# Kernel tuning notes

Hardware: AMD Instinct MI355X
Metric: run time of the kernel (lower is better)

## Reference

```python
import jax, jax.numpy as jnp
import numpy as np

BETA = 0.25

def setup_inputs() -> dict:
    key = jax.random.key(0)
    k1, k2 = jax.random.split(key)
    N, K, D = 262144, 256, 256
    z_e = jax.random.normal(k1, (N, D), dtype=jnp.float32)
    # nn.Embedding init: uniform(-1/K, 1/K)
    emb_weight = jax.random.uniform(k2, (K, D), dtype=jnp.float32, minval=-1.0 / K, maxval=1.0 / K)
    return {"z_e": z_e, "emb_weight": emb_weight}

def reference(z_e, emb_weight):
    # squared L2 distances: ||z||^2 + ||e||^2 - 2 z e^T  -> [N, K]
    dist = (jnp.sum(z_e ** 2, axis=1, keepdims=True)
            + jnp.sum(emb_weight ** 2, axis=1)
            - 2.0 * jnp.matmul(z_e, emb_weight.T))
    encoding_inds = jnp.argmin(dist, axis=1)  # [N]
    z_q = emb_weight[encoding_inds]           # [N, D]

    sg = jax.lax.stop_gradient
    commitment_loss = jnp.mean((sg(z_e) - z_q) ** 2)
    codebook_loss = jnp.mean((z_e - sg(z_q)) ** 2)
    loss = codebook_loss + BETA * commitment_loss

    # straight-through estimator
    z_q_st = z_e + sg(z_q - z_e)
    return z_q_st, encoding_inds, loss
```

## Files before the change

### kernel.cpp

```cpp
#include <hip/hip_runtime.h>

typedef __attribute__((ext_vector_type(8))) short bf16x8;
typedef __attribute__((ext_vector_type(4))) float f32x4;
typedef __attribute__((ext_vector_type(4))) unsigned short us4;
typedef __attribute__((ext_vector_type(8))) unsigned short us8;

#define NROWS 262144
#define KC 256
#define DD 256
#define BM 64
#define DK 32
#define SW 40
#define TAU 1.5e-3f
#define FCAP 65536

__device__ __forceinline__ float np_pw128_sq(const float* a) {
    float r[8];
#pragma unroll
    for (int j = 0; j < 8; ++j) r[j] = __fmul_rn(a[j], a[j]);
    for (int i = 8; i < 128; i += 8) {
#pragma unroll
        for (int j = 0; j < 8; ++j)
            r[j] = __fadd_rn(r[j], __fmul_rn(a[i + j], a[i + j]));
    }
    float t01 = __fadd_rn(r[0], r[1]), t23 = __fadd_rn(r[2], r[3]);
    float t45 = __fadd_rn(r[4], r[5]), t67 = __fadd_rn(r[6], r[7]);
    return __fadd_rn(__fadd_rn(t01, t23), __fadd_rn(t45, t67));
}
__device__ __forceinline__ float np_sum256_sq(const float* a) {
    return __fadd_rn(np_pw128_sq(a), np_pw128_sq(a + 128));
}

__device__ __forceinline__ unsigned short bf16_rne(float x) {
    unsigned b = __float_as_uint(x);
    b += 0x7FFFu + ((b >> 16) & 1u);
    return (unsigned short)(b >> 16);
}

__global__ void vq_prep(const float* __restrict__ emb, float* __restrict__ se,
                        double* __restrict__ accum, int* __restrict__ gcnt) {
    int k = threadIdx.x;
    if (k == 0) { *accum = 0.0; *gcnt = 0; }
    se[k] = np_sum256_sq(emb + (size_t)k * DD);
}

__global__ void vq_split(const float* __restrict__ emb, unsigned short* __restrict__ ph) {
    int f = (blockIdx.x * 256 + threadIdx.x) * 4;
    float4 v = *reinterpret_cast<const float4*>(emb + f);
    int k = f >> 8, d = f & 255;
    int off = (d >> 5) * (KC * DK) + k * DK + (d & 31);
    us4 h;
    h[0] = bf16_rne(v.x); h[1] = bf16_rne(v.y);
    h[2] = bf16_rne(v.z); h[3] = bf16_rne(v.w);
    *reinterpret_cast<us4*>(ph + off) = h;
}

__global__ __launch_bounds__(256)
void vq_main(const float* __restrict__ ze, const float* __restrict__ emb,
             const unsigned short* __restrict__ ph,
             const float* __restrict__ se_g, float* __restrict__ out_zq,
             float* __restrict__ out_inds, double* __restrict__ accum,
             int* __restrict__ glist, int* __restrict__ gcnt)
{
    __shared__ __attribute__((aligned(16))) unsigned short es_hi[KC * SW];
    __shared__ float  se_s[KC];
    __shared__ int    inds_s[BM];
    __shared__ float  red[256];

    const int t = threadIdx.x;
    const int w = t >> 6;
    const int l = t & 63;
    const int q = (t >> 4) & 3;
    const int c = t & 15;
    const size_t m0 = (size_t)blockIdx.x * BM;

    se_s[t] = se_g[t];

    const unsigned short* ehp0 = ph;
    us8 ereg[4];
#pragma unroll
    for (int it = 0; it < 4; ++it)
        ereg[it] = *reinterpret_cast<const us8*>(ehp0 + (it * 256 + t) * 8);

    const float* zrow = ze + (m0 + 16 * w + c) * DD + q * 8;
    float4 zlo[8], zhi[8];
#pragma unroll
    for (int dci = 0; dci < 8; ++dci) {
        zlo[dci] = *reinterpret_cast<const float4*>(zrow + dci * 32);
        zhi[dci] = *reinterpret_cast<const float4*>(zrow + dci * 32 + 4);
    }

    float sz_acc = 0.f;
    bf16x8 afrag[8];
#pragma unroll
    for (int dci = 0; dci < 8; ++dci) {
        float4 a = zlo[dci], b = zhi[dci];
        sz_acc = fmaf(a.x, a.x, sz_acc); sz_acc = fmaf(a.y, a.y, sz_acc);
        sz_acc = fmaf(a.z, a.z, sz_acc); sz_acc = fmaf(a.w, a.w, sz_acc);
        sz_acc = fmaf(b.x, b.x, sz_acc); sz_acc = fmaf(b.y, b.y, sz_acc);
        sz_acc = fmaf(b.z, b.z, sz_acc); sz_acc = fmaf(b.w, b.w, sz_acc);
        us8 h;
        h[0] = bf16_rne(a.x); h[1] = bf16_rne(a.y); h[2] = bf16_rne(a.z); h[3] = bf16_rne(a.w);
        h[4] = bf16_rne(b.x); h[5] = bf16_rne(b.y); h[6] = bf16_rne(b.z); h[7] = bf16_rne(b.w);
        afrag[dci] = __builtin_bit_cast(bf16x8, h);
    }

#pragma unroll
    for (int it = 0; it < 4; ++it) {
        int idx = it * 256 + t;
        *reinterpret_cast<us8*>(&es_hi[(idx >> 2) * SW + (idx & 3) * 8]) = ereg[it];
    }

    f32x4 acc[16];
#pragma unroll
    for (int i = 0; i < 16; ++i) acc[i] = (f32x4){0.f, 0.f, 0.f, 0.f};

#pragma unroll
    for (int dci = 0; dci < 8; ++dci) {
        __syncthreads();
        if (dci < 7) {
            const unsigned short* ehp = ph + (dci + 1) * (KC * DK);
#pragma unroll
            for (int it = 0; it < 4; ++it)
                ereg[it] = *reinterpret_cast<const us8*>(ehp + (it * 256 + t) * 8);
        }
#pragma unroll
        for (int nf = 0; nf < 16; ++nf) {
            bf16x8 b = *reinterpret_cast<const bf16x8*>(&es_hi[(16 * nf + c) * SW + q * 8]);
            acc[nf] = __builtin_amdgcn_mfma_f32_16x16x32_bf16(afrag[dci], b, acc[nf], 0, 0, 0);
        }
        __syncthreads();
        if (dci < 7) {
#pragma unroll
            for (int it = 0; it < 4; ++it) {
                int idx = it * 256 + t;
                *reinterpret_cast<us8*>(&es_hi[(idx >> 2) * SW + (idx & 3) * 8]) = ereg[it];
            }
        }
    }

    float lossv = 0.f;
#pragma unroll
    for (int j = 0; j < 4; ++j) {
        float v1 = 3.4e38f, v2 = 3.4e38f; int k1 = 0x7fffffff;
#pragma unroll
        for (int nf = 0; nf < 16; ++nf) {
            int k = 16 * nf + c;
            float dv = fmaf(-2.f, acc[nf][j], se_s[k]);
            if (dv < v1) { v2 = v1; v1 = dv; k1 = k; }
            else if (dv < v2) { v2 = dv; }
        }
#pragma unroll
        for (int off = 1; off < 16; off <<= 1) {
            float ov1 = __shfl_xor(v1, off, 64);
            float ov2 = __shfl_xor(v2, off, 64);
            int   ok1 = __shfl_xor(k1, off, 64);
            bool other = (ov1 < v1) || (ov1 == v1 && ok1 < k1);
            float nv2 = other ? fminf(v1, ov2) : fminf(v2, ov1);
            if (other) { v1 = ov1; k1 = ok1; }
            v2 = nv2;
        }
        if (c == 0) {
            int row = 16 * w + 4 * q + j;
            inds_s[row] = k1;
            lossv += v1;
            if (v2 - v1 < TAU) {
                int s = atomicAdd(gcnt, 1);
                if (s < FCAP) glist[s] = (int)(m0 + row);
            }
        }
    }
    __syncthreads();

    if (t < BM) out_inds[m0 + t] = (float)inds_s[t];

#pragma unroll
    for (int r = 0; r < 16; ++r) {
        int k = inds_s[16 * w + r];
        float4 v = *reinterpret_cast<const float4*>(emb + (size_t)k * DD + l * 4);
        *reinterpret_cast<float4*>(out_zq + (m0 + 16 * w + r) * DD + l * 4) = v;
    }

    red[t] = sz_acc + lossv;
    __syncthreads();
    for (int s = 128; s > 0; s >>= 1) {
        if (t < s) red[t] += red[t + s];
        __syncthreads();
    }
    if (t == 0) atomicAdd(accum, (double)red[0]);
}

__global__ __launch_bounds__(256)
void vq_fix(const float* __restrict__ ze, const float* __restrict__ emb,
            const float* __restrict__ se_g, const int* __restrict__ glist,
            const int* __restrict__ gcnt, float* __restrict__ out_zq,
            float* __restrict__ out_inds)
{
    __shared__ float dq[16][256];
    __shared__ float srow_s[16];
    __shared__ int   rowid_s[16];
    __shared__ int   klds[16];

    const int t = threadIdx.x;
    int F = *gcnt; if (F > FCAP) F = FCAP;
    const float se_k = se_g[t];
    const float4* e4p = reinterpret_cast<const float4*>(emb + (size_t)t * DD);

    for (int g = blockIdx.x * 16; g < F; g += gridDim.x * 16) {
        __syncthreads();
        if (t < 16) {
            int idx = g + t; if (idx > F - 1) idx = F - 1;
            int row = glist[idx];
            rowid_s[t] = row;
            srow_s[t] = np_sum256_sq(ze + (size_t)row * DD);
        }
        __syncthreads();

        const float* zp[16];
#pragma unroll
        for (int r = 0; r < 16; ++r)
            zp[r] = ze + (size_t)__builtin_amdgcn_readfirstlane(rowid_s[r]) * DD;

        float m32[16];
#pragma unroll
        for (int r = 0; r < 16; ++r) m32[r] = 0.f;
        for (int d4 = 0; d4 < 64; ++d4) {
            float4 e4 = e4p[d4];
            const int d = d4 * 4;
#pragma unroll
            for (int r = 0; r < 16; ++r) {
                m32[r] = __fmaf_rn(zp[r][d + 0], e4.x, m32[r]);
                m32[r] = __fmaf_rn(zp[r][d + 1], e4.y, m32[r]);
                m32[r] = __fmaf_rn(zp[r][d + 2], e4.z, m32[r]);
                m32[r] = __fmaf_rn(zp[r][d + 3], e4.w, m32[r]);
            }
        }
#pragma unroll
        for (int r = 0; r < 16; ++r) {
            float A = __fadd_rn(srow_s[r], se_k);
            dq[r][t] = __fsub_rn(A, __fmul_rn(2.0f, m32[r]));
        }
        __syncthreads();

        {
            const int r = t >> 4, p = t & 15;
            float bv = 3.4e38f; int bk = 0x7fffffff;
#pragma unroll
            for (int i = 0; i < 16; ++i) {
                int k = p * 16 + i;
                float v = dq[r][k];
                if (v < bv) { bv = v; bk = k; }
            }
#pragma unroll
            for (int off = 1; off < 16; off <<= 1) {
                float ov = __shfl_xor(bv, off, 64);
                int   ok = __shfl_xor(bk, off, 64);
                if (ov < bv || (ov == bv && ok < bk)) { bv = ov; bk = ok; }
            }
            if (p == 0) klds[r] = bk;
        }
        __syncthreads();

        int R = F - g; if (R > 16) R = 16;
#pragma unroll
        for (int r = 0; r < 16; ++r) {
            if (r < R) {
                int row = rowid_s[r];
                int kk  = klds[r];
                out_zq[(size_t)row * DD + t] = emb[(size_t)kk * DD + t];
                if (t == 0) out_inds[row] = (float)kk;
            }
        }
    }
}

__global__ void vq_fin(const double* __restrict__ accum, float* __restrict__ out_loss) {
    *out_loss = (float)(1.25 * (*accum) / ((double)NROWS * (double)DD));
}

extern "C" void kernel_launch(void* const* d_in, const int* in_sizes, int n_in,
                              void* d_out, int out_size, void* d_ws, size_t ws_size,
                              hipStream_t stream) {
    const float* ze  = (const float*)d_in[0];
    const float* emb = (const float*)d_in[1];
    float* out      = (float*)d_out;
    float* out_zq   = out;
    float* out_inds = out + (size_t)NROWS * DD;
    float* out_loss = out + (size_t)NROWS * DD + NROWS;

    double* accum = (double*)d_ws;
    int*    gcnt  = (int*)((char*)d_ws + 8);
    float*  se    = (float*)((char*)d_ws + 256);
    int*    glist = (int*)((char*)d_ws + 4096);
    unsigned short* ph = (unsigned short*)((char*)d_ws + 4096 + 262144);

    vq_prep<<<1, 256, 0, stream>>>(emb, se, accum, gcnt);
    vq_split<<<KC * DD / (256 * 4), 256, 0, stream>>>(emb, ph);
    vq_main<<<NROWS / BM, 256, 0, stream>>>(ze, emb, ph, se, out_zq, out_inds,
                                            accum, glist, gcnt);
    vq_fix<<<1024, 256, 0, stream>>>(ze, emb, se, glist, gcnt, out_zq, out_inds);
    vq_fin<<<1, 1, 0, stream>>>(accum, out_loss);
}
```

Baseline: 367.7 us.

## Double-buffer codebook LDS tiles and raise occupancy hint

Splits the codebook shared-memory tile into two buffers so the next chunk can be written while the current one is read, which removes one barrier per K-step. It also adds a min-blocks-per-CU hint of 3 to launch_bounds and interleaves the z loads with their conversion to shrink register live ranges. The cost is twice the LDS for the tile, and the register cap may force spills.

```diff
diff --git a/kernel.cpp b/kernel.cpp
--- a/kernel.cpp
+++ b/kernel.cpp
@@ -55,14 +55,14 @@
     *reinterpret_cast<us4*>(ph + off) = h;
 }
 
-__global__ __launch_bounds__(256)
+__global__ __launch_bounds__(256, 3)
 void vq_main(const float* __restrict__ ze, const float* __restrict__ emb,
              const unsigned short* __restrict__ ph,
              const float* __restrict__ se_g, float* __restrict__ out_zq,
              float* __restrict__ out_inds, double* __restrict__ accum,
              int* __restrict__ glist, int* __restrict__ gcnt)
 {
-    __shared__ __attribute__((aligned(16))) unsigned short es_hi[KC * SW];
+    __shared__ __attribute__((aligned(16))) unsigned short es[2][KC * SW];
     __shared__ float  se_s[KC];
     __shared__ int    inds_s[BM];
     __shared__ float  red[256];
@@ -76,39 +76,41 @@
 
     se_s[t] = se_g[t];
 
-    const unsigned short* ehp0 = ph;
     us8 ereg[4];
 #pragma unroll
     for (int it = 0; it < 4; ++it)
-        ereg[it] = *reinterpret_cast<const us8*>(ehp0 + (it * 256 + t) * 8);
+        ereg[it] = *reinterpret_cast<const us8*>(ph + (it * 256 + t) * 8);
 
     const float* zrow = ze + (m0 + 16 * w + c) * DD + q * 8;
-    float4 zlo[8], zhi[8];
-#pragma unroll
-    for (int dci = 0; dci < 8; ++dci) {
-        zlo[dci] = *reinterpret_cast<const float4*>(zrow + dci * 32);
-        zhi[dci] = *reinterpret_cast<const float4*>(zrow + dci * 32 + 4);
-    }
-
     float sz_acc = 0.f;
     bf16x8 afrag[8];
 #pragma unroll
-    for (int dci = 0; dci < 8; ++dci) {
-        float4 a = zlo[dci], b = zhi[dci];
-        sz_acc = fmaf(a.x, a.x, sz_acc); sz_acc = fmaf(a.y, a.y, sz_acc);
-        sz_acc = fmaf(a.z, a.z, sz_acc); sz_acc = fmaf(a.w, a.w, sz_acc);
-        sz_acc = fmaf(b.x, b.x, sz_acc); sz_acc = fmaf(b.y, b.y, sz_acc);
-        sz_acc = fmaf(b.z, b.z, sz_acc); sz_acc = fmaf(b.w, b.w, sz_acc);
-        us8 h;
-        h[0] = bf16_rne(a.x); h[1] = bf16_rne(a.y); h[2] = bf16_rne(a.z); h[3] = bf16_rne(a.w);
-        h[4] = bf16_rne(b.x); h[5] = bf16_rne(b.y); h[6] = bf16_rne(b.z); h[7] = bf16_rne(b.w);
-        afrag[dci] = __builtin_bit_cast(bf16x8, h);
+    for (int pp = 0; pp < 8; pp += 2) {
+        float4 a0 = *reinterpret_cast<const float4*>(zrow + pp * 32);
+        float4 b0 = *reinterpret_cast<const float4*>(zrow + pp * 32 + 4);
+        float4 a1 = *reinterpret_cast<const float4*>(zrow + pp * 32 + 32);
+        float4 b1 = *reinterpret_cast<const float4*>(zrow + pp * 32 + 36);
+        sz_acc = fmaf(a0.x, a0.x, sz_acc); sz_acc = fmaf(a0.y, a0.y, sz_acc);
+        sz_acc = fmaf(a0.z, a0.z, sz_acc); sz_acc = fmaf(a0.w, a0.w, sz_acc);
+        sz_acc = fmaf(b0.x, b0.x, sz_acc); sz_acc = fmaf(b0.y, b0.y, sz_acc);
+        sz_acc = fmaf(b0.z, b0.z, sz_acc); sz_acc = fmaf(b0.w, b0.w, sz_acc);
+        sz_acc = fmaf(a1.x, a1.x, sz_acc); sz_acc = fmaf(a1.y, a1.y, sz_acc);
+        sz_acc = fmaf(a1.z, a1.z, sz_acc); sz_acc = fmaf(a1.w, a1.w, sz_acc);
+        sz_acc = fmaf(b1.x, b1.x, sz_acc); sz_acc = fmaf(b1.y, b1.y, sz_acc);
+        sz_acc = fmaf(b1.z, b1.z, sz_acc); sz_acc = fmaf(b1.w, b1.w, sz_acc);
+        us8 h0, h1;
+        h0[0] = bf16_rne(a0.x); h0[1] = bf16_rne(a0.y); h0[2] = bf16_rne(a0.z); h0[3] = bf16_rne(a0.w);
+        h0[4] = bf16_rne(b0.x); h0[5] = bf16_rne(b0.y); h0[6] = bf16_rne(b0.z); h0[7] = bf16_rne(b0.w);
+        h1[0] = bf16_rne(a1.x); h1[1] = bf16_rne(a1.y); h1[2] = bf16_rne(a1.z); h1[3] = bf16_rne(a1.w);
+        h1[4] = bf16_rne(b1.x); h1[5] = bf16_rne(b1.y); h1[6] = bf16_rne(b1.z); h1[7] = bf16_rne(b1.w);
+        afrag[pp]     = __builtin_bit_cast(bf16x8, h0);
+        afrag[pp + 1] = __builtin_bit_cast(bf16x8, h1);
     }
 
 #pragma unroll
     for (int it = 0; it < 4; ++it) {
         int idx = it * 256 + t;
-        *reinterpret_cast<us8*>(&es_hi[(idx >> 2) * SW + (idx & 3) * 8]) = ereg[it];
+        *reinterpret_cast<us8*>(&es[0][(idx >> 2) * SW + (idx & 3) * 8]) = ereg[it];
     }
 
     f32x4 acc[16];
@@ -126,15 +128,14 @@
         }
 #pragma unroll
         for (int nf = 0; nf < 16; ++nf) {
-            bf16x8 b = *reinterpret_cast<const bf16x8*>(&es_hi[(16 * nf + c) * SW + q * 8]);
+            bf16x8 b = *reinterpret_cast<const bf16x8*>(&es[dci & 1][(16 * nf + c) * SW + q * 8]);
             acc[nf] = __builtin_amdgcn_mfma_f32_16x16x32_bf16(afrag[dci], b, acc[nf], 0, 0, 0);
         }
-        __syncthreads();
         if (dci < 7) {
 #pragma unroll
             for (int it = 0; it < 4; ++it) {
                 int idx = it * 256 + t;
-                *reinterpret_cast<us8*>(&es_hi[(idx >> 2) * SW + (idx & 3) * 8]) = ereg[it];
+                *reinterpret_cast<us8*>(&es[(dci + 1) & 1][(idx >> 2) * SW + (idx & 3) * 8]) = ereg[it];
             }
         }
     }
```

New measurement: 365.4 us. About the same (-0.6%).

## Keep codebook fragments in registers and defer z_q gather to separate kernel

Applied to the files above, without the earlier changes.

Each wave now holds a 64-code slice of the bf16 codebook in registers for the whole block, instead of streaming it through LDS with per-chunk barriers. Each block walks 128 rows in 16-row steps, prefetching the next rows' z while it runs the MFMA work. Wave-level top-2 results are merged across waves through shared memory. The z_q row gather moves out of vq_main and vq_fix into a new vq_gather kernel that reads the final indices, so vq_fix no longer writes z_q. The cost is an extra launch and a re-read of the indices, plus high register pressure from 32 bf16x8 fragments per thread under launch bounds of 2 blocks per SM.

```diff
diff --git a/kernel.cpp b/kernel.cpp
--- a/kernel.cpp
+++ b/kernel.cpp
@@ -8,9 +8,8 @@
 #define NROWS 262144
 #define KC 256
 #define DD 256
-#define BM 64
+#define BM 128
 #define DK 32
-#define SW 40
 #define TAU 1.5e-3f
 #define FCAP 65536
 
@@ -55,133 +54,126 @@
     *reinterpret_cast<us4*>(ph + off) = h;
 }
 
-__global__ __launch_bounds__(256)
-void vq_main(const float* __restrict__ ze, const float* __restrict__ emb,
-             const unsigned short* __restrict__ ph,
-             const float* __restrict__ se_g, float* __restrict__ out_zq,
-             float* __restrict__ out_inds, double* __restrict__ accum,
-             int* __restrict__ glist, int* __restrict__ gcnt)
+__global__ __launch_bounds__(256, 2)
+void vq_main(const float* __restrict__ ze, const unsigned short* __restrict__ ph,
+             const float* __restrict__ se_g, float* __restrict__ out_inds,
+             double* __restrict__ accum, int* __restrict__ glist, int* __restrict__ gcnt)
 {
-    __shared__ __attribute__((aligned(16))) unsigned short es_hi[KC * SW];
-    __shared__ float  se_s[KC];
-    __shared__ int    inds_s[BM];
-    __shared__ float  red[256];
+    __shared__ float se_s[KC];
+    __shared__ float wv1[4 * 16], wv2[4 * 16];
+    __shared__ int   wk1[4 * 16];
+    __shared__ float red[256];
 
     const int t = threadIdx.x;
     const int w = t >> 6;
-    const int l = t & 63;
     const int q = (t >> 4) & 3;
     const int c = t & 15;
     const size_t m0 = (size_t)blockIdx.x * BM;
 
     se_s[t] = se_g[t];
 
-    const unsigned short* ehp0 = ph;
-    us8 ereg[4];
-#pragma unroll
-    for (int it = 0; it < 4; ++it)
-        ereg[it] = *reinterpret_cast<const us8*>(ehp0 + (it * 256 + t) * 8);
-
-    const float* zrow = ze + (m0 + 16 * w + c) * DD + q * 8;
-    float4 zlo[8], zhi[8];
-#pragma unroll
-    for (int dci = 0; dci < 8; ++dci) {
-        zlo[dci] = *reinterpret_cast<const float4*>(zrow + dci * 32);
-        zhi[dci] = *reinterpret_cast<const float4*>(zrow + dci * 32 + 4);
-    }
-
-    float sz_acc = 0.f;
-    bf16x8 afrag[8];
-#pragma unroll
-    for (int dci = 0; dci < 8; ++dci) {
-        float4 a = zlo[dci], b = zhi[dci];
-        sz_acc = fmaf(a.x, a.x, sz_acc); sz_acc = fmaf(a.y, a.y, sz_acc);
-        sz_acc = fmaf(a.z, a.z, sz_acc); sz_acc = fmaf(a.w, a.w, sz_acc);
-        sz_acc = fmaf(b.x, b.x, sz_acc); sz_acc = fmaf(b.y, b.y, sz_acc);
-        sz_acc = fmaf(b.z, b.z, sz_acc); sz_acc = fmaf(b.w, b.w, sz_acc);
-        us8 h;
-        h[0] = bf16_rne(a.x); h[1] = bf16_rne(a.y); h[2] = bf16_rne(a.z); h[3] = bf16_rne(a.w);
-        h[4] = bf16_rne(b.x); h[5] = bf16_rne(b.y); h[6] = bf16_rne(b.z); h[7] = bf16_rne(b.w);
-        afrag[dci] = __builtin_bit_cast(bf16x8, h);
-    }
-
-#pragma unroll
-    for (int it = 0; it < 4; ++it) {
-        int idx = it * 256 + t;
-        *reinterpret_cast<us8*>(&es_hi[(idx >> 2) * SW + (idx & 3) * 8]) = ereg[it];
-    }
-
-    f32x4 acc[16];
-#pragma unroll
-    for (int i = 0; i < 16; ++i) acc[i] = (f32x4){0.f, 0.f, 0.f, 0.f};
-
-#pragma unroll
-    for (int dci = 0; dci < 8; ++dci) {
-        __syncthreads();
-        if (dci < 7) {
-            const unsigned short* ehp = ph + (dci + 1) * (KC * DK);
-#pragma unroll
-            for (int it = 0; it < 4; ++it)
-                ereg[it] = *reinterpret_cast<const us8*>(ehp + (it * 256 + t) * 8);
-        }
-#pragma unroll
-        for (int nf = 0; nf < 16; ++nf) {
-            bf16x8 b = *reinterpret_cast<const bf16x8*>(&es_hi[(16 * nf + c) * SW + q * 8]);
-            acc[nf] = __builtin_amdgcn_mfma_f32_16x16x32_bf16(afrag[dci], b, acc[nf], 0, 0, 0);
-        }
-        __syncthreads();
-        if (dci < 7) {
-#pragma unroll
-            for (int it = 0; it < 4; ++it) {
-                int idx = it * 256 + t;
-                *reinterpret_cast<us8*>(&es_hi[(idx >> 2) * SW + (idx & 3) * 8]) = ereg[it];
-            }
-        }
-    }
-
-    float lossv = 0.f;
-#pragma unroll
-    for (int j = 0; j < 4; ++j) {
-        float v1 = 3.4e38f, v2 = 3.4e38f; int k1 = 0x7fffffff;
-#pragma unroll
-        for (int nf = 0; nf < 16; ++nf) {
-            int k = 16 * nf + c;
-            float dv = fmaf(-2.f, acc[nf][j], se_s[k]);
-            if (dv < v1) { v2 = v1; v1 = dv; k1 = k; }
-            else if (dv < v2) { v2 = dv; }
-        }
-#pragma unroll
-        for (int off = 1; off < 16; off <<= 1) {
-            float ov1 = __shfl_xor(v1, off, 64);
-            float ov2 = __shfl_xor(v2, off, 64);
-            int   ok1 = __shfl_xor(k1, off, 64);
-            bool other = (ov1 < v1) || (ov1 == v1 && ok1 < k1);
-            float nv2 = other ? fminf(v1, ov2) : fminf(v2, ov1);
-            if (other) { v1 = ov1; k1 = ok1; }
-            v2 = nv2;
-        }
-        if (c == 0) {
-            int row = 16 * w + 4 * q + j;
-            inds_s[row] = k1;
-            lossv += v1;
+    bf16x8 bfr[4][8];
+#pragma unroll
+    for (int nf = 0; nf < 4; ++nf)
+#pragma unroll
+        for (int dci = 0; dci < 8; ++dci)
+            bfr[nf][dci] = *reinterpret_cast<const bf16x8*>(
+                ph + dci * (KC * DK) + (w * 64 + nf * 16 + c) * DK + q * 8);
+
+    __syncthreads();
+
+    float sz_run = 0.f, loss_run = 0.f;
+
+    float4 z0[8], z1[8];
+    {
+        const float* zb = ze + (m0 + c) * DD + q * 8;
+#pragma unroll
+        for (int dci = 0; dci < 8; ++dci) {
+            z0[dci] = *reinterpret_cast<const float4*>(zb + dci * 32);
+            z1[dci] = *reinterpret_cast<const float4*>(zb + dci * 32 + 4);
+        }
+    }
+
+    for (int step = 0; step < BM / 16; ++step) {
+        f32x4 acc[4];
+#pragma unroll
+        for (int nf = 0; nf < 4; ++nf) acc[nf] = (f32x4){0.f, 0.f, 0.f, 0.f};
+#pragma unroll
+        for (int dci = 0; dci < 8; ++dci) {
+            float4 a = z0[dci], b = z1[dci];
+            if (w == 0) {
+                sz_run = fmaf(a.x, a.x, sz_run); sz_run = fmaf(a.y, a.y, sz_run);
+                sz_run = fmaf(a.z, a.z, sz_run); sz_run = fmaf(a.w, a.w, sz_run);
+                sz_run = fmaf(b.x, b.x, sz_run); sz_run = fmaf(b.y, b.y, sz_run);
+                sz_run = fmaf(b.z, b.z, sz_run); sz_run = fmaf(b.w, b.w, sz_run);
+            }
+            us8 h;
+            h[0] = bf16_rne(a.x); h[1] = bf16_rne(a.y); h[2] = bf16_rne(a.z); h[3] = bf16_rne(a.w);
+            h[4] = bf16_rne(b.x); h[5] = bf16_rne(b.y); h[6] = bf16_rne(b.z); h[7] = bf16_rne(b.w);
+            bf16x8 af = __builtin_bit_cast(bf16x8, h);
+#pragma unroll
+            for (int nf = 0; nf < 4; ++nf)
+                acc[nf] = __builtin_amdgcn_mfma_f32_16x16x32_bf16(af, bfr[nf][dci], acc[nf], 0, 0, 0);
+        }
+        if (step < BM / 16 - 1) {
+            const float* zb = ze + (m0 + (step + 1) * 16 + c) * DD + q * 8;
+#pragma unroll
+            for (int dci = 0; dci < 8; ++dci) {
+                z0[dci] = *reinterpret_cast<const float4*>(zb + dci * 32);
+                z1[dci] = *reinterpret_cast<const float4*>(zb + dci * 32 + 4);
+            }
+        }
+
+#pragma unroll
+        for (int j = 0; j < 4; ++j) {
+            float v1 = 3.4e38f, v2 = 3.4e38f; int k1 = 0x7fffffff;
+#pragma unroll
+            for (int nf = 0; nf < 4; ++nf) {
+                int k = 64 * w + 16 * nf + c;
+                float dv = fmaf(-2.f, acc[nf][j], se_s[k]);
+                if (dv < v1) { v2 = v1; v1 = dv; k1 = k; }
+                else if (dv < v2) { v2 = dv; }
+            }
+#pragma unroll
+            for (int off = 1; off < 16; off <<= 1) {
+                float ov1 = __shfl_xor(v1, off, 64);
+                float ov2 = __shfl_xor(v2, off, 64);
+                int   ok1 = __shfl_xor(k1, off, 64);
+                bool other = (ov1 < v1) || (ov1 == v1 && ok1 < k1);
+                float nv2 = other ? fminf(v1, ov2) : fminf(v2, ov1);
+                if (other) { v1 = ov1; k1 = ok1; }
+                v2 = nv2;
+            }
+            if (c == 0) {
+                wv1[w * 16 + 4 * q + j] = v1;
+                wv2[w * 16 + 4 * q + j] = v2;
+                wk1[w * 16 + 4 * q + j] = k1;
+            }
+        }
+        __syncthreads();
+
+        if (t < 16) {
+            float v1 = wv1[t], v2 = wv2[t]; int k1 = wk1[t];
+#pragma unroll
+            for (int ww = 1; ww < 4; ++ww) {
+                float ov1 = wv1[ww * 16 + t], ov2 = wv2[ww * 16 + t];
+                int ok1 = wk1[ww * 16 + t];
+                bool other = (ov1 < v1) || (ov1 == v1 && ok1 < k1);
+                float nv2 = other ? fminf(v1, ov2) : fminf(v2, ov1);
+                if (other) { v1 = ov1; k1 = ok1; }
+                v2 = nv2;
+            }
+            out_inds[m0 + step * 16 + t] = (float)k1;
+            loss_run += v1;
             if (v2 - v1 < TAU) {
-                int s = atomicAdd(gcnt, 1);
-                if (s < FCAP) glist[s] = (int)(m0 + row);
-            }
-        }
-    }
-    __syncthreads();
-
-    if (t < BM) out_inds[m0 + t] = (float)inds_s[t];
-
-#pragma unroll
-    for (int r = 0; r < 16; ++r) {
-        int k = inds_s[16 * w + r];
-        float4 v = *reinterpret_cast<const float4*>(emb + (size_t)k * DD + l * 4);
-        *reinterpret_cast<float4*>(out_zq + (m0 + 16 * w + r) * DD + l * 4) = v;
-    }
-
-    red[t] = sz_acc + lossv;
+                int s_ = atomicAdd(gcnt, 1);
+                if (s_ < FCAP) glist[s_] = (int)(m0 + step * 16 + t);
+            }
+        }
+        __syncthreads();
+    }
+
+    red[t] = (w == 0 ? sz_run : 0.f) + (t < 16 ? loss_run : 0.f);
     __syncthreads();
     for (int s = 128; s > 0; s >>= 1) {
         if (t < s) red[t] += red[t + s];
@@ -193,13 +185,11 @@
 __global__ __launch_bounds__(256)
 void vq_fix(const float* __restrict__ ze, const float* __restrict__ emb,
             const float* __restrict__ se_g, const int* __restrict__ glist,
-            const int* __restrict__ gcnt, float* __restrict__ out_zq,
-            float* __restrict__ out_inds)
+            const int* __restrict__ gcnt, float* __restrict__ out_inds)
 {
     __shared__ float dq[16][256];
     __shared__ float srow_s[16];
     __shared__ int   rowid_s[16];
-    __shared__ int   klds[16];
 
     const int t = threadIdx.x;
     int F = *gcnt; if (F > FCAP) F = FCAP;
@@ -257,20 +247,24 @@
                 int   ok = __shfl_xor(bk, off, 64);
                 if (ov < bv || (ov == bv && ok < bk)) { bv = ov; bk = ok; }
             }
-            if (p == 0) klds[r] = bk;
-        }
-        __syncthreads();
-
-        int R = F - g; if (R > 16) R = 16;
-#pragma unroll
-        for (int r = 0; r < 16; ++r) {
-            if (r < R) {
-                int row = rowid_s[r];
-                int kk  = klds[r];
-                out_zq[(size_t)row * DD + t] = emb[(size_t)kk * DD + t];
-                if (t == 0) out_inds[row] = (float)kk;
-            }
-        }
+            if (p == 0 && g + r < F) out_inds[rowid_s[r]] = (float)bk;
+        }
+        __syncthreads();
+    }
+}
+
+__global__ __launch_bounds__(256)
+void vq_gather(const float* __restrict__ emb, const float* __restrict__ out_inds,
+               float* __restrict__ out_zq)
+{
+    const int t = threadIdx.x;
+    const int w = t >> 6, l = t & 63;
+    const size_t m0 = (size_t)blockIdx.x * 128 + (size_t)w * 32;
+#pragma unroll 8
+    for (int r = 0; r < 32; ++r) {
+        int k = (int)out_inds[m0 + r];
+        float4 v = *reinterpret_cast<const float4*>(emb + (size_t)k * DD + l * 4);
+        *reinterpret_cast<float4*>(out_zq + (m0 + r) * DD + l * 4) = v;
     }
 }
 
@@ -296,8 +290,8 @@
 
     vq_prep<<<1, 256, 0, stream>>>(emb, se, accum, gcnt);
     vq_split<<<KC * DD / (256 * 4), 256, 0, stream>>>(emb, ph);
-    vq_main<<<NROWS / BM, 256, 0, stream>>>(ze, emb, ph, se, out_zq, out_inds,
-                                            accum, glist, gcnt);
-    vq_fix<<<1024, 256, 0, stream>>>(ze, emb, se, glist, gcnt, out_zq, out_inds);
+    vq_main<<<NROWS / BM, 256, 0, stream>>>(ze, ph, se, out_inds, accum, glist, gcnt);
+    vq_fix<<<1024, 256, 0, stream>>>(ze, emb, se, glist, gcnt, out_inds);
+    vq_gather<<<NROWS / 128, 256, 0, stream>>>(emb, out_inds, out_zq);
     vq_fin<<<1, 1, 0, stream>>>(accum, out_loss);
 }
```

After: 347.6 us. 5.5% less time.
